# Kernel optimization log

Hardware: AMD Instinct MI355X
Metric: run time of the kernel (lower is better)

## Reference

```python
import jax, jax.numpy as jnp
import numpy as np

D_MODEL = 1024
NUM_HEADS = 16
D_K = D_MODEL // NUM_HEADS


def setup_inputs() -> dict:
    key = jax.random.key(0)
    ks = jax.random.split(key, 9)
    s = 1.0 / np.sqrt(D_MODEL)
    X = jax.random.normal(ks[0], (4, 2048, D_MODEL), dtype=jnp.float32)
    Wq = jax.random.uniform(ks[1], (D_MODEL, D_MODEL), jnp.float32, -s, s)
    bq = jax.random.uniform(ks[2], (D_MODEL,), jnp.float32, -s, s)
    Wk = jax.random.uniform(ks[3], (D_MODEL, D_MODEL), jnp.float32, -s, s)
    bk = jax.random.uniform(ks[4], (D_MODEL,), jnp.float32, -s, s)
    Wv = jax.random.uniform(ks[5], (D_MODEL, D_MODEL), jnp.float32, -s, s)
    bv = jax.random.uniform(ks[6], (D_MODEL,), jnp.float32, -s, s)
    Wo = jax.random.uniform(ks[7], (D_MODEL, D_MODEL), jnp.float32, -s, s)
    bo = jax.random.uniform(ks[8], (D_MODEL,), jnp.float32, -s, s)
    return {"X": X, "Wq": Wq, "bq": bq, "Wk": Wk, "bk": bk,
            "Wv": Wv, "bv": bv, "Wo": Wo, "bo": bo}


def reference(X, Wq, bq, Wk, bk, Wv, bv, Wo, bo):
    B, n, d = X.shape
    # Linear layers: y = x @ W^T + b (torch Linear convention)
    Q = X @ Wq.T + bq
    K = X @ Wk.T + bk
    V = X @ Wv.T + bv
    # [B, n, H, d_k] -> [B, H, n, d_k]
    Q = Q.reshape(B, n, NUM_HEADS, D_K).transpose(0, 2, 1, 3)
    K = K.reshape(B, n, NUM_HEADS, D_K).transpose(0, 2, 1, 3)
    V = V.reshape(B, n, NUM_HEADS, D_K).transpose(0, 2, 1, 3)
    scores = jnp.einsum('bhqd,bhkd->bhqk', Q, K) / jnp.sqrt(jnp.float32(D_K))
    attn = jax.nn.softmax(scores, axis=-1)  # [B, H, n, n]
    out = jnp.einsum('bhqk,bhkd->bhqd', attn, V)
    out = out.transpose(0, 2, 1, 3).reshape(B, n, d)
    return out @ Wo.T + bo
```

## Files before the change

kernel.cpp:

```cpp
#include <hip/hip_runtime.h>
#include <hip/hip_bf16.h>
#include <stdint.h>

typedef __hip_bfloat16 bf16;
typedef __bf16 bf16x8 __attribute__((ext_vector_type(8)));
typedef float floatx4 __attribute__((ext_vector_type(4)));

#define MFMA16(a, b, c) __builtin_amdgcn_mfma_f32_16x16x32_bf16((a), (b), (c), 0, 0, 0)

typedef __attribute__((address_space(3))) uint32_t lds_u32;
typedef const __attribute__((address_space(1))) uint32_t gbl_u32;

__device__ __forceinline__ void async16(const void* g, void* s) {
    __builtin_amdgcn_global_load_lds((gbl_u32*)g, (lds_u32*)s, 16, 0, 0);
}

__device__ __forceinline__ unsigned short f2bf_rne(float f) {
    union { float f; unsigned u; } v; v.f = f;
    const unsigned u = v.u;
    return (unsigned short)((u + 0x7FFFu + ((u >> 16) & 1u)) >> 16);
}
__device__ __forceinline__ unsigned pk2(float a, float b) {
    __hip_bfloat162 h = __float22bfloat162_rn(make_float2(a, b));
    return *(unsigned*)&h;
}

#define A_X   0L
#define A_WQ  8388608L
#define A_WK  9437184L
#define A_WV  10485760L
#define A_WO  11534336L
#define A_END 12582912L

__global__ __launch_bounds__(256) void cvt5(
    const float* __restrict__ s0, const float* __restrict__ s1,
    const float* __restrict__ s2, const float* __restrict__ s3,
    const float* __restrict__ s4, unsigned short* __restrict__ dst)
{
    const long beg[6] = {A_X, A_WQ, A_WK, A_WV, A_WO, A_END};
    const float* srcs[5] = {s0, s1, s2, s3, s4};
    const long nchunk = A_END / 8;
    for (long c = (long)blockIdx.x * 256 + threadIdx.x; c < nchunk;
         c += (long)gridDim.x * 256) {
        const long off = c * 8;
        int s = 0;
#pragma unroll
        for (int i = 1; i < 5; ++i) if (off >= beg[i]) s = i;
        const float* sp = srcs[s] + (off - beg[s]);
        const uint4 lo = *(const uint4*)(sp);
        const uint4 hi = *(const uint4*)(sp + 4);
        const float* fl = (const float*)&lo;
        const float* fh = (const float*)&hi;
        uint4 o;
        o.x = pk2(fl[0], fl[1]); o.y = pk2(fl[2], fl[3]);
        o.z = pk2(fh[0], fh[1]); o.w = pk2(fh[2], fh[3]);
        *(uint4*)(dst + off) = o;
    }
}

template <int CFP32, int TRANSV>
__global__ __launch_bounds__(256, 2) void gemm_bt3(
    const bf16* __restrict__ A,
    const bf16* __restrict__ W0, const bf16* __restrict__ W1, const bf16* __restrict__ W2,
    const float* __restrict__ b0, const float* __restrict__ b1, const float* __restrict__ b2,
    void* __restrict__ C0, void* __restrict__ C1, void* __restrict__ C2)
{
    __shared__ bf16 As[128 * 64];
    __shared__ bf16 Bs[128 * 64];

    const int tid = threadIdx.x;
    const int which = blockIdx.y >> 3;
    const int nt = blockIdx.y & 7;
    const bf16* __restrict__ W   = (which == 0) ? W0 : ((which == 1) ? W1 : W2);
    const float* __restrict__ bb = (which == 0) ? b0 : ((which == 1) ? b1 : b2);
    void* __restrict__ C         = (which == 0) ? C0 : ((which == 1) ? C1 : C2);

    const int m0 = blockIdx.x * 128;
    const int n0 = nt * 128;

    const int w  = tid >> 6;
    const int l  = tid & 63;
    const int lr = l & 15;
    const int q  = l >> 4;
    const int wm = (w & 1) * 64;
    const int wn = (w >> 1) * 64;
    const int wbase = tid & 0xC0;

    floatx4 acc[4][4];
#pragma unroll
    for (int i = 0; i < 4; ++i)
#pragma unroll
        for (int j = 0; j < 4; ++j)
            acc[i][j] = (floatx4){0.f, 0.f, 0.f, 0.f};

#pragma unroll 1
    for (int kt = 0; kt < 16; ++kt) {
        __syncthreads();
#pragma unroll
        for (int r = 0; r < 4; ++r) {
            const int u   = r * 256 + tid;
            const int row = u >> 3;
            const int kg  = u & 7;
            const int kgg = kg ^ (row & 7);
            const size_t goffA = (size_t)(m0 + row) * 1024 + kt * 64 + kgg * 8;
            const size_t goffB = (size_t)(n0 + row) * 1024 + kt * 64 + kgg * 8;
            bf16* dA = As + (size_t)(r * 256 + wbase) * 8;
            bf16* dB = Bs + (size_t)(r * 256 + wbase) * 8;
            async16(A + goffA, dA);
            async16(W + goffB, dB);
        }
        asm volatile("s_waitcnt vmcnt(0)" ::: "memory");
        __syncthreads();

#pragma unroll
        for (int ks = 0; ks < 2; ++ks) {
            bf16x8 av[4], bv[4];
#pragma unroll
            for (int i = 0; i < 4; ++i) {
                const int row = wm + i * 16 + lr;
                const int kg  = (ks * 4 + q) ^ (row & 7);
                av[i] = *(const bf16x8*)(As + row * 64 + kg * 8);
            }
#pragma unroll
            for (int j = 0; j < 4; ++j) {
                const int row = wn + j * 16 + lr;
                const int kg  = (ks * 4 + q) ^ (row & 7);
                bv[j] = *(const bf16x8*)(Bs + row * 64 + kg * 8);
            }
#pragma unroll
            for (int i = 0; i < 4; ++i)
#pragma unroll
                for (int j = 0; j < 4; ++j)
                    acc[i][j] = MFMA16(av[i], bv[j], acc[i][j]);
        }
    }

    if (TRANSV && which == 2) {
#pragma unroll
        for (int j = 0; j < 4; ++j) {
            const int col = n0 + wn + j * 16 + lr;
            const float bj = bb[col];
            const int h = col >> 6, d = col & 63;
#pragma unroll
            for (int i = 0; i < 4; ++i) {
                const int row0 = m0 + wm + i * 16 + q * 4;
                const int b = row0 >> 11;
                const int key = row0 & 2047;
                uint2 ov;
                ov.x = pk2(acc[i][j][0] + bj, acc[i][j][1] + bj);
                ov.y = pk2(acc[i][j][2] + bj, acc[i][j][3] + bj);
                *(uint2*)((unsigned short*)C +
                          ((size_t)(b * 16 + h) * 64 + d) * 2048 + key) = ov;
            }
        }
    } else {
#pragma unroll
        for (int j = 0; j < 4; ++j) {
            const int col = n0 + wn + j * 16 + lr;
            const float bj = bb[col];
#pragma unroll
            for (int i = 0; i < 4; ++i) {
#pragma unroll
                for (int r = 0; r < 4; ++r) {
                    const int row = m0 + wm + i * 16 + q * 4 + r;
                    const float val = acc[i][j][r] + bj;
                    if (CFP32)
                        ((float*)C)[(long)row * 1024 + col] = val;
                    else
                        ((unsigned short*)C)[(long)row * 1024 + col] = f2bf_rne(val);
                }
            }
        }
    }
}

__device__ __forceinline__ int swzk(int R) {
    return (R & 7) ^ (((R >> 3) & 1) << 2);
}

__global__ __launch_bounds__(256, 2) void attn_flash(
    const bf16* __restrict__ Q, const bf16* __restrict__ K, const bf16* __restrict__ VT,
    bf16* __restrict__ AO)
{
    __shared__ bf16 Ks[2][64 * 64];
    __shared__ bf16 Vt[2][64 * 64];

    const int tid = threadIdx.x;
    const int b = blockIdx.y >> 4, h = blockIdx.y & 15;
    const int q0 = blockIdx.x * 128;
    const size_t base = ((size_t)b * 2048) * 1024 + (size_t)h * 64;
    const size_t vtb  = (size_t)(b * 16 + h) * 64 * 2048;

    const int w  = tid >> 6;
    const int l  = tid & 63;
    const int lr = l & 15;
    const int q  = l >> 4;

    const int krow = tid >> 3, kkg = tid & 7;
    const int vd = tid >> 2,   vko = tid & 3;
    const int ksw = kkg ^ swzk(krow);

    bf16x8 qb[2][2];
#pragma unroll
    for (int i = 0; i < 2; ++i)
#pragma unroll
        for (int ks = 0; ks < 2; ++ks)
            qb[i][ks] = *(const bf16x8*)(Q + base +
                (size_t)(q0 + w * 32 + i * 16 + lr) * 1024 + ks * 32 + q * 8);

    uint4 kreg0 = *(const uint4*)(K + base + (size_t)krow * 1024 + kkg * 8);
    uint4 kreg1 = *(const uint4*)(K + base + (size_t)(32 + krow) * 1024 + kkg * 8);
    uint4 vreg0 = *(const uint4*)(VT + vtb + (size_t)vd * 2048 + vko * 8);
    uint4 vreg1 = *(const uint4*)(VT + vtb + (size_t)vd * 2048 + 32 + vko * 8);

    floatx4 O[2][4];
#pragma unroll
    for (int i = 0; i < 2; ++i)
#pragma unroll
        for (int d = 0; d < 4; ++d) O[i][d] = (floatx4){0.f, 0.f, 0.f, 0.f};
    float mprev[2] = {-1e30f, -1e30f}, lsum[2] = {0.f, 0.f};
    const float cs = 0.18033688011112042f;

#pragma unroll 1
    for (int kt = 0; kt < 32; ++kt) {
        bf16* __restrict__ Kc = Ks[kt & 1];
        bf16* __restrict__ Vc = Vt[kt & 1];

        *(uint4*)(Kc + krow * 64 + ksw * 8)                          = kreg0;
        *(uint4*)(Kc + (32 + krow) * 64 + ksw * 8)                   = kreg1;
        *(uint4*)(Vc + vd * 64 + ((vko ^ (vd & 7)) * 8))             = vreg0;
        *(uint4*)(Vc + vd * 64 + (((4 + vko) ^ (vd & 7)) * 8))       = vreg1;
        __syncthreads();

        if (kt < 31) {
            const size_t kb_ = base + (size_t)((kt + 1) * 64) * 1024;
            kreg0 = *(const uint4*)(K + kb_ + (size_t)krow * 1024 + kkg * 8);
            kreg1 = *(const uint4*)(K + kb_ + (size_t)(32 + krow) * 1024 + kkg * 8);
            const size_t vb2 = vtb + (size_t)vd * 2048 + (kt + 1) * 64;
            vreg0 = *(const uint4*)(VT + vb2 + vko * 8);
            vreg1 = *(const uint4*)(VT + vb2 + 32 + vko * 8);
        }

        floatx4 s[2][4];
#pragma unroll
        for (int i = 0; i < 2; ++i)
#pragma unroll
            for (int t = 0; t < 4; ++t)
                s[i][t] = (floatx4){0.f, 0.f, 0.f, 0.f};
#pragma unroll
        for (int ks = 0; ks < 2; ++ks) {
            bf16x8 kb[4];
#pragma unroll
            for (int t = 0; t < 4; ++t) {
                const int R = (t & 1) * 32 + (t >> 1) * 4 + (lr >> 2) * 8 + (lr & 3);
                kb[t] = *(const bf16x8*)(Kc + R * 64 +
                                         (((ks * 4 + q) ^ swzk(R)) * 8));
            }
            __builtin_amdgcn_s_setprio(1);
#pragma unroll
            for (int i = 0; i < 2; ++i)
#pragma unroll
                for (int t = 0; t < 4; ++t)
                    s[i][t] = MFMA16(kb[t], qb[i][ks], s[i][t]);
            __builtin_amdgcn_s_setprio(0);
        }

#pragma unroll
        for (int i = 0; i < 2; ++i) {
            float t0 = fmaxf(fmaxf(s[i][0][0], s[i][0][1]), s[i][0][2]);
            float t1 = fmaxf(fmaxf(s[i][0][3], s[i][1][0]), s[i][1][1]);
            float t2 = fmaxf(fmaxf(s[i][1][2], s[i][1][3]), s[i][2][0]);
            float t3 = fmaxf(fmaxf(s[i][2][1], s[i][2][2]), s[i][2][3]);
            float t4 = fmaxf(fmaxf(s[i][3][0], s[i][3][1]), s[i][3][2]);
            const float vm = fmaxf(fmaxf(fmaxf(t0, t1), fmaxf(t2, t3)),
                                   fmaxf(t4, s[i][3][3]));
            const float mt = vm * cs;
            if (__any(mt > mprev[i] + 8.f)) {
                float vr = fmaxf(mt, __shfl_xor(mt, 16));
                vr = fmaxf(vr, __shfl_xor(vr, 32));
                const float mnew  = fmaxf(mprev[i], vr);
                const float alpha = exp2f(mprev[i] - mnew);
                mprev[i] = mnew;
                lsum[i] *= alpha;
#pragma unroll
                for (int d = 0; d < 4; ++d) O[i][d] *= alpha;
            }
            const float mcur = mprev[i];
            float rsum = 0.f;
#pragma unroll
            for (int t = 0; t < 4; ++t)
#pragma unroll
                for (int r = 0; r < 4; ++r) {
                    const float p = exp2f(s[i][t][r] * cs - mcur);
                    s[i][t][r] = p;
                    rsum += p;
                }
            lsum[i] += rsum;
        }

#pragma unroll
        for (int kc = 0; kc < 2; ++kc) {
            bf16x8 va[4];
#pragma unroll
            for (int dt = 0; dt < 4; ++dt) {
                const int R = dt * 16 + lr;
                va[dt] = *(const bf16x8*)(Vc + R * 64 +
                                          (((kc * 4 + q) ^ (R & 7)) * 8));
            }
            bf16x8 pb[2];
#pragma unroll
            for (int i = 0; i < 2; ++i) {
                union { uint4 u; bf16x8 v; } pw;
                pw.u.x = pk2(s[i][kc][0], s[i][kc][1]);
                pw.u.y = pk2(s[i][kc][2], s[i][kc][3]);
                pw.u.z = pk2(s[i][kc + 2][0], s[i][kc + 2][1]);
                pw.u.w = pk2(s[i][kc + 2][2], s[i][kc + 2][3]);
                pb[i] = pw.v;
            }
            __builtin_amdgcn_s_setprio(1);
#pragma unroll
            for (int i = 0; i < 2; ++i)
#pragma unroll
                for (int dt = 0; dt < 4; ++dt)
                    O[i][dt] = MFMA16(va[dt], pb[i], O[i][dt]);
            __builtin_amdgcn_s_setprio(0);
        }
    }

#pragma unroll
    for (int i = 0; i < 2; ++i) {
        float ls = lsum[i];
        ls += __shfl_xor(ls, 16);
        ls += __shfl_xor(ls, 32);
        const float inv = 1.f / ls;
        const int row = q0 + w * 32 + i * 16 + lr;
#pragma unroll
        for (int dt = 0; dt < 4; ++dt) {
            uint2 oh;
            oh.x = pk2(O[i][dt][0] * inv, O[i][dt][1] * inv);
            oh.y = pk2(O[i][dt][2] * inv, O[i][dt][3] * inv);
            *(uint2*)((unsigned short*)AO + base + (size_t)row * 1024 +
                      dt * 16 + q * 4) = oh;
        }
    }
}

extern "C" void kernel_launch(void* const* d_in, const int* in_sizes, int n_in,
                              void* d_out, int out_size, void* d_ws, size_t ws_size,
                              hipStream_t stream) {
    (void)in_sizes; (void)n_in; (void)out_size; (void)ws_size;
    const float* X  = (const float*)d_in[0];
    const float* Wq = (const float*)d_in[1];
    const float* bq = (const float*)d_in[2];
    const float* Wk = (const float*)d_in[3];
    const float* bk = (const float*)d_in[4];
    const float* Wv = (const float*)d_in[5];
    const float* bv = (const float*)d_in[6];
    const float* Wo = (const float*)d_in[7];
    const float* bo = (const float*)d_in[8];
    float* out = (float*)d_out;

    unsigned short* arena = (unsigned short*)d_ws;
    bf16* Xb  = (bf16*)(arena + A_X);
    bf16* Wqb = (bf16*)(arena + A_WQ);
    bf16* Wkb = (bf16*)(arena + A_WK);
    bf16* Wvb = (bf16*)(arena + A_WV);
    bf16* Wob = (bf16*)(arena + A_WO);

    const size_t SZ = (size_t)8192 * 1024;
    bf16* Qb  = (bf16*)(arena + A_END);
    bf16* Kb  = Qb + SZ;
    bf16* VTb = Kb + SZ;
    bf16* AOb = VTb + SZ;

    cvt5<<<dim3(1536), dim3(256), 0, stream>>>(X, Wq, Wk, Wv, Wo, arena);

    gemm_bt3<0, 1><<<dim3(64, 24), dim3(256), 0, stream>>>(
        Xb, Wqb, Wkb, Wvb, bq, bk, bv, (void*)Qb, (void*)Kb, (void*)VTb);

    attn_flash<<<dim3(16, 64), dim3(256), 0, stream>>>(Qb, Kb, VTb, AOb);

    gemm_bt3<1, 0><<<dim3(64, 8), dim3(256), 0, stream>>>(
        AOb, Wob, Wob, Wob, bo, bo, bo, (void*)out, (void*)out, (void*)out);
}
```

Baseline: 294.2 us.

## Restructure flash attention loop to interleave softmax with PV MFMAs and defer LDS stores

The attention kernel's main loop is rescheduled. LDS stores for the next K/V tile now happen at the end of the iteration instead of before the barrier, and global prefetches are issued unconditionally with a clamped index. The two query sub-tiles' softmax and PV MFMAs are interleaved so exp work for one overlaps matrix ops for the other. The running-max rescale check is merged into a single branch, and the hardware exp2 intrinsic replaces exp2f. This aims to hide LDS and VALU latency behind MFMA work, at the cost of more live registers and a redundant final prefetch.

```diff
diff --git a/kernel.cpp b/kernel.cpp
--- a/kernel.cpp
+++ b/kernel.cpp
@@ -182,8 +182,8 @@
     const bf16* __restrict__ Q, const bf16* __restrict__ K, const bf16* __restrict__ VT,
     bf16* __restrict__ AO)
 {
-    __shared__ bf16 Ks[2][64 * 64];
-    __shared__ bf16 Vt[2][64 * 64];
+    __shared__ bf16 Ks[2 * 64 * 64];
+    __shared__ bf16 Vt[2 * 64 * 64];
 
     const int tid = threadIdx.x;
     const int b = blockIdx.y >> 4, h = blockIdx.y & 15;
@@ -200,6 +200,11 @@
     const int vd = tid >> 2,   vko = tid & 3;
     const int ksw = kkg ^ swzk(krow);
 
+    const int stK0 = krow * 64 + ksw * 8;
+    const int stK1 = (32 + krow) * 64 + ksw * 8;
+    const int stV0 = vd * 64 + ((vko ^ (vd & 7)) * 8);
+    const int stV1 = vd * 64 + (((4 + vko) ^ (vd & 7)) * 8);
+
     bf16x8 qb[2][2];
 #pragma unroll
     for (int i = 0; i < 2; ++i)
@@ -212,133 +217,190 @@
     uint4 kreg1 = *(const uint4*)(K + base + (size_t)(32 + krow) * 1024 + kkg * 8);
     uint4 vreg0 = *(const uint4*)(VT + vtb + (size_t)vd * 2048 + vko * 8);
     uint4 vreg1 = *(const uint4*)(VT + vtb + (size_t)vd * 2048 + 32 + vko * 8);
-
-    floatx4 O[2][4];
-#pragma unroll
-    for (int i = 0; i < 2; ++i)
-#pragma unroll
-        for (int d = 0; d < 4; ++d) O[i][d] = (floatx4){0.f, 0.f, 0.f, 0.f};
-    float mprev[2] = {-1e30f, -1e30f}, lsum[2] = {0.f, 0.f};
+    *(uint4*)(Ks + stK0) = kreg0;
+    *(uint4*)(Ks + stK1) = kreg1;
+    *(uint4*)(Vt + stV0) = vreg0;
+    *(uint4*)(Vt + stV1) = vreg1;
+
+    floatx4 O0[4], O1[4];
+#pragma unroll
+    for (int d = 0; d < 4; ++d) {
+        O0[d] = (floatx4){0.f, 0.f, 0.f, 0.f};
+        O1[d] = (floatx4){0.f, 0.f, 0.f, 0.f};
+    }
+    float m0 = -1e30f, m1 = -1e30f, ls0 = 0.f, ls1 = 0.f;
     const float cs = 0.18033688011112042f;
 
 #pragma unroll 1
     for (int kt = 0; kt < 32; ++kt) {
-        bf16* __restrict__ Kc = Ks[kt & 1];
-        bf16* __restrict__ Vc = Vt[kt & 1];
-
-        *(uint4*)(Kc + krow * 64 + ksw * 8)                          = kreg0;
-        *(uint4*)(Kc + (32 + krow) * 64 + ksw * 8)                   = kreg1;
-        *(uint4*)(Vc + vd * 64 + ((vko ^ (vd & 7)) * 8))             = vreg0;
-        *(uint4*)(Vc + vd * 64 + (((4 + vko) ^ (vd & 7)) * 8))       = vreg1;
         __syncthreads();
-
-        if (kt < 31) {
-            const size_t kb_ = base + (size_t)((kt + 1) * 64) * 1024;
-            kreg0 = *(const uint4*)(K + kb_ + (size_t)krow * 1024 + kkg * 8);
-            kreg1 = *(const uint4*)(K + kb_ + (size_t)(32 + krow) * 1024 + kkg * 8);
-            const size_t vb2 = vtb + (size_t)vd * 2048 + (kt + 1) * 64;
-            vreg0 = *(const uint4*)(VT + vb2 + vko * 8);
-            vreg1 = *(const uint4*)(VT + vb2 + 32 + vko * 8);
-        }
-
-        floatx4 s[2][4];
-#pragma unroll
-        for (int i = 0; i < 2; ++i)
-#pragma unroll
-            for (int t = 0; t < 4; ++t)
-                s[i][t] = (floatx4){0.f, 0.f, 0.f, 0.f};
+        const int bsel = (kt & 1) * 4096;
+        const int bnxt = 4096 - bsel;
+
+        const int ktn = (kt < 31) ? (kt + 1) : 31;
+        const size_t kb_ = base + (size_t)ktn * 65536;
+        kreg0 = *(const uint4*)(K + kb_ + (size_t)krow * 1024 + kkg * 8);
+        kreg1 = *(const uint4*)(K + kb_ + (size_t)(32 + krow) * 1024 + kkg * 8);
+        const size_t vb2 = vtb + (size_t)vd * 2048 + (size_t)ktn * 64;
+        vreg0 = *(const uint4*)(VT + vb2 + vko * 8);
+        vreg1 = *(const uint4*)(VT + vb2 + 32 + vko * 8);
+
+        floatx4 s0[4], s1[4];
+#pragma unroll
+        for (int t = 0; t < 4; ++t) {
+            s0[t] = (floatx4){0.f, 0.f, 0.f, 0.f};
+            s1[t] = (floatx4){0.f, 0.f, 0.f, 0.f};
+        }
 #pragma unroll
         for (int ks = 0; ks < 2; ++ks) {
             bf16x8 kb[4];
 #pragma unroll
             for (int t = 0; t < 4; ++t) {
                 const int R = (t & 1) * 32 + (t >> 1) * 4 + (lr >> 2) * 8 + (lr & 3);
-                kb[t] = *(const bf16x8*)(Kc + R * 64 +
+                kb[t] = *(const bf16x8*)(Ks + bsel + R * 64 +
                                          (((ks * 4 + q) ^ swzk(R)) * 8));
             }
             __builtin_amdgcn_s_setprio(1);
 #pragma unroll
-            for (int i = 0; i < 2; ++i)
-#pragma unroll
-                for (int t = 0; t < 4; ++t)
-                    s[i][t] = MFMA16(kb[t], qb[i][ks], s[i][t]);
+            for (int t = 0; t < 4; ++t) s0[t] = MFMA16(kb[t], qb[0][ks], s0[t]);
+#pragma unroll
+            for (int t = 0; t < 4; ++t) s1[t] = MFMA16(kb[t], qb[1][ks], s1[t]);
             __builtin_amdgcn_s_setprio(0);
         }
 
-#pragma unroll
-        for (int i = 0; i < 2; ++i) {
-            float t0 = fmaxf(fmaxf(s[i][0][0], s[i][0][1]), s[i][0][2]);
-            float t1 = fmaxf(fmaxf(s[i][0][3], s[i][1][0]), s[i][1][1]);
-            float t2 = fmaxf(fmaxf(s[i][1][2], s[i][1][3]), s[i][2][0]);
-            float t3 = fmaxf(fmaxf(s[i][2][1], s[i][2][2]), s[i][2][3]);
-            float t4 = fmaxf(fmaxf(s[i][3][0], s[i][3][1]), s[i][3][2]);
-            const float vm = fmaxf(fmaxf(fmaxf(t0, t1), fmaxf(t2, t3)),
-                                   fmaxf(t4, s[i][3][3]));
-            const float mt = vm * cs;
-            if (__any(mt > mprev[i] + 8.f)) {
-                float vr = fmaxf(mt, __shfl_xor(mt, 16));
-                vr = fmaxf(vr, __shfl_xor(vr, 32));
-                const float mnew  = fmaxf(mprev[i], vr);
-                const float alpha = exp2f(mprev[i] - mnew);
-                mprev[i] = mnew;
-                lsum[i] *= alpha;
-#pragma unroll
-                for (int d = 0; d < 4; ++d) O[i][d] *= alpha;
-            }
-            const float mcur = mprev[i];
-            float rsum = 0.f;
-#pragma unroll
-            for (int t = 0; t < 4; ++t)
-#pragma unroll
-                for (int r = 0; r < 4; ++r) {
-                    const float p = exp2f(s[i][t][r] * cs - mcur);
-                    s[i][t][r] = p;
-                    rsum += p;
-                }
-            lsum[i] += rsum;
-        }
-
+        float a0 = fmaxf(fmaxf(s0[0][0], s0[0][1]), s0[0][2]);
+        float a1 = fmaxf(fmaxf(s0[0][3], s0[1][0]), s0[1][1]);
+        float a2 = fmaxf(fmaxf(s0[1][2], s0[1][3]), s0[2][0]);
+        float a3 = fmaxf(fmaxf(s0[2][1], s0[2][2]), s0[2][3]);
+        float a4 = fmaxf(fmaxf(s0[3][0], s0[3][1]), s0[3][2]);
+        const float mt0 = fmaxf(fmaxf(fmaxf(a0, a1), fmaxf(a2, a3)),
+                                fmaxf(a4, s0[3][3])) * cs;
+        float c0 = fmaxf(fmaxf(s1[0][0], s1[0][1]), s1[0][2]);
+        float c1 = fmaxf(fmaxf(s1[0][3], s1[1][0]), s1[1][1]);
+        float c2 = fmaxf(fmaxf(s1[1][2], s1[1][3]), s1[2][0]);
+        float c3 = fmaxf(fmaxf(s1[2][1], s1[2][2]), s1[2][3]);
+        float c4 = fmaxf(fmaxf(s1[3][0], s1[3][1]), s1[3][2]);
+        const float mt1 = fmaxf(fmaxf(fmaxf(c0, c1), fmaxf(c2, c3)),
+                                fmaxf(c4, s1[3][3])) * cs;
+
+        if (__any((mt0 > m0 + 8.f) || (mt1 > m1 + 8.f))) {
+            float vr0 = fmaxf(mt0, __shfl_xor(mt0, 16));
+            vr0 = fmaxf(vr0, __shfl_xor(vr0, 32));
+            const float mn0 = fmaxf(m0, vr0);
+            const float al0 = __builtin_amdgcn_exp2f(m0 - mn0);
+            m0 = mn0; ls0 *= al0;
+#pragma unroll
+            for (int d = 0; d < 4; ++d) O0[d] *= al0;
+            float vr1 = fmaxf(mt1, __shfl_xor(mt1, 16));
+            vr1 = fmaxf(vr1, __shfl_xor(vr1, 32));
+            const float mn1 = fmaxf(m1, vr1);
+            const float al1 = __builtin_amdgcn_exp2f(m1 - mn1);
+            m1 = mn1; ls1 *= al1;
+#pragma unroll
+            for (int d = 0; d < 4; ++d) O1[d] *= al1;
+        }
+
+        bf16x8 va0[4];
+#pragma unroll
+        for (int dt = 0; dt < 4; ++dt) {
+            const int R = dt * 16 + lr;
+            va0[dt] = *(const bf16x8*)(Vt + bsel + R * 64 + ((q ^ (R & 7)) * 8));
+        }
+
+#pragma unroll
+        for (int t = 0; t < 4; ++t)
+#pragma unroll
+            for (int r = 0; r < 4; ++r)
+                s0[t][r] = __builtin_amdgcn_exp2f(s0[t][r] * cs - m0);
+        {
+            floatx4 rs = (s0[0] + s0[1]) + (s0[2] + s0[3]);
+            ls0 += (rs[0] + rs[1]) + (rs[2] + rs[3]);
+        }
+        bf16x8 pb0[2];
 #pragma unroll
         for (int kc = 0; kc < 2; ++kc) {
-            bf16x8 va[4];
-#pragma unroll
-            for (int dt = 0; dt < 4; ++dt) {
-                const int R = dt * 16 + lr;
-                va[dt] = *(const bf16x8*)(Vc + R * 64 +
-                                          (((kc * 4 + q) ^ (R & 7)) * 8));
-            }
-            bf16x8 pb[2];
-#pragma unroll
-            for (int i = 0; i < 2; ++i) {
-                union { uint4 u; bf16x8 v; } pw;
-                pw.u.x = pk2(s[i][kc][0], s[i][kc][1]);
-                pw.u.y = pk2(s[i][kc][2], s[i][kc][3]);
-                pw.u.z = pk2(s[i][kc + 2][0], s[i][kc + 2][1]);
-                pw.u.w = pk2(s[i][kc + 2][2], s[i][kc + 2][3]);
-                pb[i] = pw.v;
-            }
-            __builtin_amdgcn_s_setprio(1);
-#pragma unroll
-            for (int i = 0; i < 2; ++i)
-#pragma unroll
-                for (int dt = 0; dt < 4; ++dt)
-                    O[i][dt] = MFMA16(va[dt], pb[i], O[i][dt]);
-            __builtin_amdgcn_s_setprio(0);
-        }
-    }
-
-#pragma unroll
-    for (int i = 0; i < 2; ++i) {
-        float ls = lsum[i];
+            union { uint4 u; bf16x8 v; } pw;
+            pw.u.x = pk2(s0[kc][0], s0[kc][1]);
+            pw.u.y = pk2(s0[kc][2], s0[kc][3]);
+            pw.u.z = pk2(s0[kc + 2][0], s0[kc + 2][1]);
+            pw.u.w = pk2(s0[kc + 2][2], s0[kc + 2][3]);
+            pb0[kc] = pw.v;
+        }
+
+        __builtin_amdgcn_s_setprio(1);
+#pragma unroll
+        for (int dt = 0; dt < 4; ++dt) O0[dt] = MFMA16(va0[dt], pb0[0], O0[dt]);
+        __builtin_amdgcn_s_setprio(0);
+
+        bf16x8 va1[4];
+#pragma unroll
+        for (int dt = 0; dt < 4; ++dt) {
+            const int R = dt * 16 + lr;
+            va1[dt] = *(const bf16x8*)(Vt + bsel + R * 64 +
+                                       (((4 + q) ^ (R & 7)) * 8));
+        }
+
+#pragma unroll
+        for (int t = 0; t < 4; ++t)
+#pragma unroll
+            for (int r = 0; r < 4; ++r)
+                s1[t][r] = __builtin_amdgcn_exp2f(s1[t][r] * cs - m1);
+        {
+            floatx4 rs = (s1[0] + s1[1]) + (s1[2] + s1[3]);
+            ls1 += (rs[0] + rs[1]) + (rs[2] + rs[3]);
+        }
+        bf16x8 pb1[2];
+#pragma unroll
+        for (int kc = 0; kc < 2; ++kc) {
+            union { uint4 u; bf16x8 v; } pw;
+            pw.u.x = pk2(s1[kc][0], s1[kc][1]);
+            pw.u.y = pk2(s1[kc][2], s1[kc][3]);
+            pw.u.z = pk2(s1[kc + 2][0], s1[kc + 2][1]);
+            pw.u.w = pk2(s1[kc + 2][2], s1[kc + 2][3]);
+            pb1[kc] = pw.v;
+        }
+
+        __builtin_amdgcn_s_setprio(1);
+#pragma unroll
+        for (int dt = 0; dt < 4; ++dt) O0[dt] = MFMA16(va1[dt], pb0[1], O0[dt]);
+#pragma unroll
+        for (int dt = 0; dt < 4; ++dt) O1[dt] = MFMA16(va0[dt], pb1[0], O1[dt]);
+#pragma unroll
+        for (int dt = 0; dt < 4; ++dt) O1[dt] = MFMA16(va1[dt], pb1[1], O1[dt]);
+        __builtin_amdgcn_s_setprio(0);
+
+        *(uint4*)(Ks + bnxt + stK0) = kreg0;
+        *(uint4*)(Ks + bnxt + stK1) = kreg1;
+        *(uint4*)(Vt + bnxt + stV0) = vreg0;
+        *(uint4*)(Vt + bnxt + stV1) = vreg1;
+    }
+
+    {
+        float ls = ls0;
         ls += __shfl_xor(ls, 16);
         ls += __shfl_xor(ls, 32);
         const float inv = 1.f / ls;
-        const int row = q0 + w * 32 + i * 16 + lr;
+        const int row = q0 + w * 32 + lr;
 #pragma unroll
         for (int dt = 0; dt < 4; ++dt) {
             uint2 oh;
-            oh.x = pk2(O[i][dt][0] * inv, O[i][dt][1] * inv);
-            oh.y = pk2(O[i][dt][2] * inv, O[i][dt][3] * inv);
+            oh.x = pk2(O0[dt][0] * inv, O0[dt][1] * inv);
+            oh.y = pk2(O0[dt][2] * inv, O0[dt][3] * inv);
+            *(uint2*)((unsigned short*)AO + base + (size_t)row * 1024 +
+                      dt * 16 + q * 4) = oh;
+        }
+    }
+    {
+        float ls = ls1;
+        ls += __shfl_xor(ls, 16);
+        ls += __shfl_xor(ls, 32);
+        const float inv = 1.f / ls;
+        const int row = q0 + w * 32 + 16 + lr;
+#pragma unroll
+        for (int dt = 0; dt < 4; ++dt) {
+            uint2 oh;
+            oh.x = pk2(O1[dt][0] * inv, O1[dt][1] * inv);
+            oh.y = pk2(O1[dt][2] * inv, O1[dt][3] * inv);
             *(uint2*)((unsigned short*)AO + base + (size_t)row * 1024 +
                       dt * 16 + q * 4) = oh;
         }
```

Result: faster. 276.0 us, median of 3 (-6.2%).

## Restructure attention kernel to 8 waves with 16 query rows each

Applied to the files above, without the earlier changes.

The flash attention kernel now launches 512 threads per block (8 waves), and each wave handles 16 query rows instead of 32. Per-thread register state (Q fragments, O accumulators, K/V staging) is halved to allow more resident waves. The K/V prefetch for the next tile is now written to the alternate LDS buffer at the end of each iteration, so one barrier per tile suffices. It also switches to the raw exp2 builtin and keeps a vector row-sum. The trade-off is that each K/V tile loaded into LDS is reused by fewer rows per wave, adding LDS read traffic per MFMA.

```diff
diff --git a/kernel.cpp b/kernel.cpp
--- a/kernel.cpp
+++ b/kernel.cpp
@@ -178,12 +178,12 @@
     return (R & 7) ^ (((R >> 3) & 1) << 2);
 }
 
-__global__ __launch_bounds__(256, 2) void attn_flash(
+__global__ __launch_bounds__(512, 4) void attn_flash(
     const bf16* __restrict__ Q, const bf16* __restrict__ K, const bf16* __restrict__ VT,
     bf16* __restrict__ AO)
 {
-    __shared__ bf16 Ks[2][64 * 64];
-    __shared__ bf16 Vt[2][64 * 64];
+    __shared__ bf16 Ks[2 * 64 * 64];
+    __shared__ bf16 Vt[2 * 64 * 64];
 
     const int tid = threadIdx.x;
     const int b = blockIdx.y >> 4, h = blockIdx.y & 15;
@@ -196,149 +196,123 @@
     const int lr = l & 15;
     const int q  = l >> 4;
 
-    const int krow = tid >> 3, kkg = tid & 7;
-    const int vd = tid >> 2,   vko = tid & 3;
-    const int ksw = kkg ^ swzk(krow);
-
-    bf16x8 qb[2][2];
-#pragma unroll
-    for (int i = 0; i < 2; ++i)
-#pragma unroll
-        for (int ks = 0; ks < 2; ++ks)
-            qb[i][ks] = *(const bf16x8*)(Q + base +
-                (size_t)(q0 + w * 32 + i * 16 + lr) * 1024 + ks * 32 + q * 8);
-
-    uint4 kreg0 = *(const uint4*)(K + base + (size_t)krow * 1024 + kkg * 8);
-    uint4 kreg1 = *(const uint4*)(K + base + (size_t)(32 + krow) * 1024 + kkg * 8);
-    uint4 vreg0 = *(const uint4*)(VT + vtb + (size_t)vd * 2048 + vko * 8);
-    uint4 vreg1 = *(const uint4*)(VT + vtb + (size_t)vd * 2048 + 32 + vko * 8);
-
-    floatx4 O[2][4];
-#pragma unroll
-    for (int i = 0; i < 2; ++i)
-#pragma unroll
-        for (int d = 0; d < 4; ++d) O[i][d] = (floatx4){0.f, 0.f, 0.f, 0.f};
-    float mprev[2] = {-1e30f, -1e30f}, lsum[2] = {0.f, 0.f};
+    const int srow = tid >> 3;
+    const int soct = tid & 7;
+    const int stK = srow * 64 + ((soct ^ swzk(srow)) * 8);
+    const int stV = srow * 64 + ((soct ^ (srow & 7)) * 8);
+
+    bf16x8 qb[2];
+#pragma unroll
+    for (int ks = 0; ks < 2; ++ks)
+        qb[ks] = *(const bf16x8*)(Q + base +
+            (size_t)(q0 + w * 16 + lr) * 1024 + ks * 32 + q * 8);
+
+    uint4 kreg = *(const uint4*)(K + base + (size_t)srow * 1024 + soct * 8);
+    uint4 vreg = *(const uint4*)(VT + vtb + (size_t)srow * 2048 + soct * 8);
+    *(uint4*)(Ks + stK) = kreg;
+    *(uint4*)(Vt + stV) = vreg;
+
+    const floatx4 z4 = (floatx4){0.f, 0.f, 0.f, 0.f};
+    floatx4 O[4];
+#pragma unroll
+    for (int d = 0; d < 4; ++d) O[d] = z4;
+    float m0 = -1e30f;
+    floatx4 lsv = z4;
     const float cs = 0.18033688011112042f;
 
 #pragma unroll 1
     for (int kt = 0; kt < 32; ++kt) {
-        bf16* __restrict__ Kc = Ks[kt & 1];
-        bf16* __restrict__ Vc = Vt[kt & 1];
-
-        *(uint4*)(Kc + krow * 64 + ksw * 8)                          = kreg0;
-        *(uint4*)(Kc + (32 + krow) * 64 + ksw * 8)                   = kreg1;
-        *(uint4*)(Vc + vd * 64 + ((vko ^ (vd & 7)) * 8))             = vreg0;
-        *(uint4*)(Vc + vd * 64 + (((4 + vko) ^ (vd & 7)) * 8))       = vreg1;
         __syncthreads();
-
-        if (kt < 31) {
-            const size_t kb_ = base + (size_t)((kt + 1) * 64) * 1024;
-            kreg0 = *(const uint4*)(K + kb_ + (size_t)krow * 1024 + kkg * 8);
-            kreg1 = *(const uint4*)(K + kb_ + (size_t)(32 + krow) * 1024 + kkg * 8);
-            const size_t vb2 = vtb + (size_t)vd * 2048 + (kt + 1) * 64;
-            vreg0 = *(const uint4*)(VT + vb2 + vko * 8);
-            vreg1 = *(const uint4*)(VT + vb2 + 32 + vko * 8);
-        }
-
-        floatx4 s[2][4];
-#pragma unroll
-        for (int i = 0; i < 2; ++i)
-#pragma unroll
-            for (int t = 0; t < 4; ++t)
-                s[i][t] = (floatx4){0.f, 0.f, 0.f, 0.f};
-#pragma unroll
-        for (int ks = 0; ks < 2; ++ks) {
-            bf16x8 kb[4];
-#pragma unroll
-            for (int t = 0; t < 4; ++t) {
-                const int R = (t & 1) * 32 + (t >> 1) * 4 + (lr >> 2) * 8 + (lr & 3);
-                kb[t] = *(const bf16x8*)(Kc + R * 64 +
-                                         (((ks * 4 + q) ^ swzk(R)) * 8));
-            }
-            __builtin_amdgcn_s_setprio(1);
-#pragma unroll
-            for (int i = 0; i < 2; ++i)
-#pragma unroll
-                for (int t = 0; t < 4; ++t)
-                    s[i][t] = MFMA16(kb[t], qb[i][ks], s[i][t]);
-            __builtin_amdgcn_s_setprio(0);
-        }
-
-#pragma unroll
-        for (int i = 0; i < 2; ++i) {
-            float t0 = fmaxf(fmaxf(s[i][0][0], s[i][0][1]), s[i][0][2]);
-            float t1 = fmaxf(fmaxf(s[i][0][3], s[i][1][0]), s[i][1][1]);
-            float t2 = fmaxf(fmaxf(s[i][1][2], s[i][1][3]), s[i][2][0]);
-            float t3 = fmaxf(fmaxf(s[i][2][1], s[i][2][2]), s[i][2][3]);
-            float t4 = fmaxf(fmaxf(s[i][3][0], s[i][3][1]), s[i][3][2]);
-            const float vm = fmaxf(fmaxf(fmaxf(t0, t1), fmaxf(t2, t3)),
-                                   fmaxf(t4, s[i][3][3]));
-            const float mt = vm * cs;
-            if (__any(mt > mprev[i] + 8.f)) {
-                float vr = fmaxf(mt, __shfl_xor(mt, 16));
-                vr = fmaxf(vr, __shfl_xor(vr, 32));
-                const float mnew  = fmaxf(mprev[i], vr);
-                const float alpha = exp2f(mprev[i] - mnew);
-                mprev[i] = mnew;
-                lsum[i] *= alpha;
-#pragma unroll
-                for (int d = 0; d < 4; ++d) O[i][d] *= alpha;
-            }
-            const float mcur = mprev[i];
-            float rsum = 0.f;
-#pragma unroll
-            for (int t = 0; t < 4; ++t)
-#pragma unroll
-                for (int r = 0; r < 4; ++r) {
-                    const float p = exp2f(s[i][t][r] * cs - mcur);
-                    s[i][t][r] = p;
-                    rsum += p;
-                }
-            lsum[i] += rsum;
-        }
-
+        const int bsel = (kt & 1) * 4096;
+        const int bnxt = 4096 - bsel;
+
+        const int ktn = (kt < 31) ? (kt + 1) : 31;
+        kreg = *(const uint4*)(K + base + (size_t)ktn * 65536 +
+                               (size_t)srow * 1024 + soct * 8);
+        vreg = *(const uint4*)(VT + vtb + (size_t)srow * 2048 +
+                               (size_t)ktn * 64 + soct * 8);
+
+        bf16x8 kb0[4], kb1[4];
+#pragma unroll
+        for (int t = 0; t < 4; ++t) {
+            const int R = (t & 1) * 32 + (t >> 1) * 4 + (lr >> 2) * 8 + (lr & 3);
+            kb0[t] = *(const bf16x8*)(Ks + bsel + R * 64 + ((q ^ swzk(R)) * 8));
+            kb1[t] = *(const bf16x8*)(Ks + bsel + R * 64 + (((4 + q) ^ swzk(R)) * 8));
+        }
+        floatx4 s[4];
+        __builtin_amdgcn_s_setprio(1);
+#pragma unroll
+        for (int t = 0; t < 4; ++t) s[t] = MFMA16(kb0[t], qb[0], z4);
+#pragma unroll
+        for (int t = 0; t < 4; ++t) s[t] = MFMA16(kb1[t], qb[1], s[t]);
+        __builtin_amdgcn_s_setprio(0);
+
+        float a0 = fmaxf(fmaxf(s[0][0], s[0][1]), s[0][2]);
+        float a1 = fmaxf(fmaxf(s[0][3], s[1][0]), s[1][1]);
+        float a2 = fmaxf(fmaxf(s[1][2], s[1][3]), s[2][0]);
+        float a3 = fmaxf(fmaxf(s[2][1], s[2][2]), s[2][3]);
+        float a4 = fmaxf(fmaxf(s[3][0], s[3][1]), s[3][2]);
+        const float mt = fmaxf(fmaxf(fmaxf(a0, a1), fmaxf(a2, a3)),
+                               fmaxf(a4, s[3][3])) * cs;
+
+        if (__any(mt > m0 + 8.f)) {
+            float vr = fmaxf(mt, __shfl_xor(mt, 16));
+            vr = fmaxf(vr, __shfl_xor(vr, 32));
+            const float mn = fmaxf(m0, vr);
+            const float al = __builtin_amdgcn_exp2f(m0 - mn);
+            m0 = mn; lsv *= al;
+#pragma unroll
+            for (int d = 0; d < 4; ++d) O[d] *= al;
+        }
+
+        bf16x8 va0[4], va1[4];
+#pragma unroll
+        for (int dt = 0; dt < 4; ++dt) {
+            const int R = dt * 16 + lr;
+            va0[dt] = *(const bf16x8*)(Vt + bsel + R * 64 + ((q ^ (R & 7)) * 8));
+            va1[dt] = *(const bf16x8*)(Vt + bsel + R * 64 +
+                                       (((4 + q) ^ (R & 7)) * 8));
+        }
+
+#pragma unroll
+        for (int t = 0; t < 4; ++t)
+#pragma unroll
+            for (int r = 0; r < 4; ++r)
+                s[t][r] = __builtin_amdgcn_exp2f(s[t][r] * cs - m0);
+        lsv += (s[0] + s[1]) + (s[2] + s[3]);
+        bf16x8 pb[2];
 #pragma unroll
         for (int kc = 0; kc < 2; ++kc) {
-            bf16x8 va[4];
-#pragma unroll
-            for (int dt = 0; dt < 4; ++dt) {
-                const int R = dt * 16 + lr;
-                va[dt] = *(const bf16x8*)(Vc + R * 64 +
-                                          (((kc * 4 + q) ^ (R & 7)) * 8));
-            }
-            bf16x8 pb[2];
-#pragma unroll
-            for (int i = 0; i < 2; ++i) {
-                union { uint4 u; bf16x8 v; } pw;
-                pw.u.x = pk2(s[i][kc][0], s[i][kc][1]);
-                pw.u.y = pk2(s[i][kc][2], s[i][kc][3]);
-                pw.u.z = pk2(s[i][kc + 2][0], s[i][kc + 2][1]);
-                pw.u.w = pk2(s[i][kc + 2][2], s[i][kc + 2][3]);
-                pb[i] = pw.v;
-            }
-            __builtin_amdgcn_s_setprio(1);
-#pragma unroll
-            for (int i = 0; i < 2; ++i)
-#pragma unroll
-                for (int dt = 0; dt < 4; ++dt)
-                    O[i][dt] = MFMA16(va[dt], pb[i], O[i][dt]);
-            __builtin_amdgcn_s_setprio(0);
-        }
-    }
-
-#pragma unroll
-    for (int i = 0; i < 2; ++i) {
-        float ls = lsum[i];
+            union { uint4 u; bf16x8 v; } pw;
+            pw.u.x = pk2(s[kc][0], s[kc][1]);
+            pw.u.y = pk2(s[kc][2], s[kc][3]);
+            pw.u.z = pk2(s[kc + 2][0], s[kc + 2][1]);
+            pw.u.w = pk2(s[kc + 2][2], s[kc + 2][3]);
+            pb[kc] = pw.v;
+        }
+
+        __builtin_amdgcn_s_setprio(1);
+#pragma unroll
+        for (int dt = 0; dt < 4; ++dt) O[dt] = MFMA16(va0[dt], pb[0], O[dt]);
+#pragma unroll
+        for (int dt = 0; dt < 4; ++dt) O[dt] = MFMA16(va1[dt], pb[1], O[dt]);
+        __builtin_amdgcn_s_setprio(0);
+
+        *(uint4*)(Ks + bnxt + stK) = kreg;
+        *(uint4*)(Vt + bnxt + stV) = vreg;
+    }
+
+    {
+        float ls = (lsv[0] + lsv[1]) + (lsv[2] + lsv[3]);
         ls += __shfl_xor(ls, 16);
         ls += __shfl_xor(ls, 32);
         const float inv = 1.f / ls;
-        const int row = q0 + w * 32 + i * 16 + lr;
+        const int row = q0 + w * 16 + lr;
 #pragma unroll
         for (int dt = 0; dt < 4; ++dt) {
             uint2 oh;
-            oh.x = pk2(O[i][dt][0] * inv, O[i][dt][1] * inv);
-            oh.y = pk2(O[i][dt][2] * inv, O[i][dt][3] * inv);
+            oh.x = pk2(O[dt][0] * inv, O[dt][1] * inv);
+            oh.y = pk2(O[dt][2] * inv, O[dt][3] * inv);
             *(uint2*)((unsigned short*)AO + base + (size_t)row * 1024 +
                       dt * 16 + q * 4) = oh;
         }
@@ -378,7 +352,7 @@
     gemm_bt3<0, 1><<<dim3(64, 24), dim3(256), 0, stream>>>(
         Xb, Wqb, Wkb, Wvb, bq, bk, bv, (void*)Qb, (void*)Kb, (void*)VTb);
 
-    attn_flash<<<dim3(16, 64), dim3(256), 0, stream>>>(Qb, Kb, VTb, AOb);
+    attn_flash<<<dim3(16, 64), dim3(512), 0, stream>>>(Qb, Kb, VTb, AOb);
 
     gemm_bt3<1, 0><<<dim3(64, 8), dim3(256), 0, stream>>>(
         AOb, Wob, Wob, Wob, bo, bo, bo, (void*)out, (void*)out, (void*)out);
```

Result: faster. 264.7 us (-10.0%).
